# Kernel optimization log

Measured on AMD Instinct MI355X. Metric: run time of the kernel, lower is better.

The kernel has to match this reference:

```python
import jax, jax.numpy as jnp
import numpy as np

ALLOWED_BORDER = 0
CLOBBER_POSITIVES = False
NEG_OVERLAP = 0.3
POS_OVERLAP = 0.7
STRIDE = 16


def _mkanchors(ws, hs, cx, cy):
    return np.stack([cx - 0.5 * (ws - 1), cy - 0.5 * (hs - 1),
                     cx + 0.5 * (ws - 1), cy + 0.5 * (hs - 1)], axis=1)


def _base_anchors(base_size=16, ratios=(0.5, 1.0, 2.0), scales=(8, 16, 32)):
    ratios = np.asarray(ratios, dtype=np.float64)
    scales = np.asarray(scales, dtype=np.float64)
    w = h = float(base_size)
    cx = cy = 0.5 * (base_size - 1)
    size = w * h
    ws = np.round(np.sqrt(size / ratios))
    hs = np.round(ws * ratios)
    ratio_anchors = _mkanchors(ws, hs, cx, cy)  # (3,4)
    out = []
    for x1, y1, x2, y2 in ratio_anchors:
        aw = x2 - x1 + 1
        ah = y2 - y1 + 1
        acx = x1 + 0.5 * (aw - 1)
        acy = y1 + 0.5 * (ah - 1)
        out.append(_mkanchors(aw * scales, ah * scales, acx, acy))
    return np.concatenate(out, axis=0).astype(np.float32)  # (9,4)


def _shift(rr, cc, stride):
    # keras_rcnn.backend.shift: grid of shifted base anchors, (rr*cc*9, 4)
    base = _base_anchors()
    sx = np.arange(rr) * stride
    sy = np.arange(cc) * stride
    SX, SY = np.meshgrid(sx, sy)
    shifts = np.stack([SX.ravel(), SY.ravel(), SX.ravel(), SY.ravel()], axis=1).astype(np.float32)
    return jnp.asarray((shifts[:, None, :] + base[None, :, :]).reshape(-1, 4))


def _iou(a, b):
    # pairwise IoU, (A,4) x (G,4) -> (A,G); +1 pixel convention as in keras-rcnn overlap()
    area_a = (a[:, 2] - a[:, 0] + 1.0) * (a[:, 3] - a[:, 1] + 1.0)
    area_b = (b[:, 2] - b[:, 0] + 1.0) * (b[:, 3] - b[:, 1] + 1.0)
    iw = jnp.maximum(jnp.minimum(a[:, None, 2], b[None, :, 2]) - jnp.maximum(a[:, None, 0], b[None, :, 0]) + 1.0, 0.0)
    ih = jnp.maximum(jnp.minimum(a[:, None, 3], b[None, :, 3]) - jnp.maximum(a[:, None, 1], b[None, :, 1]) + 1.0, 0.0)
    inter = iw * ih
    union = jnp.maximum(area_a[:, None] + area_b[None, :] - inter, 1e-8)
    return inter / union


def _bbox_transform(ex, gt):
    ew = ex[:, 2] - ex[:, 0] + 1.0
    eh = ex[:, 3] - ex[:, 1] + 1.0
    ecx = ex[:, 0] + 0.5 * ew
    ecy = ex[:, 1] + 0.5 * eh
    gw = gt[:, 2] - gt[:, 0] + 1.0
    gh = gt[:, 3] - gt[:, 1] + 1.0
    gcx = gt[:, 0] + 0.5 * gw
    gcy = gt[:, 1] + 0.5 * gh
    return jnp.stack([(gcx - ecx) / ew, (gcy - ecy) / eh,
                      jnp.log(gw / ew), jnp.log(gh / eh)], axis=1)


def setup_inputs():
    key = jax.random.key(0)
    k1, k2, k3 = jax.random.split(key, 3)
    rr = cc = 128
    ch = 18  # 2 * 9 anchors
    G = 256
    H = W = 2048.0
    scores = jax.random.normal(k1, (1, rr, cc, ch), dtype=jnp.float32)
    xy = jax.random.uniform(k2, (1, G, 2), minval=0.0, maxval=1700.0)
    wh = jax.random.uniform(k3, (1, G, 2), minval=16.0, maxval=300.0)
    gt_boxes = jnp.concatenate([xy, xy + wh], axis=-1).astype(jnp.float32)
    metadata = jnp.array([[H, W, 1.0]], dtype=jnp.float32)
    return {"scores": scores, "gt_boxes": gt_boxes, "metadata": metadata}


def reference(scores, gt_boxes, metadata):
    meta = metadata[0, :]
    gt = gt_boxes[0]  # (G,4)
    rr, cc, ch = scores.shape[1:]
    anchors = _shift(rr, cc, STRIDE)  # (A,4), A = rr*cc*9
    # inside_image mask (keeps static shapes: mask instead of gather, unmap at end)
    inside = ((anchors[:, 0] >= -ALLOWED_BORDER) & (anchors[:, 1] >= -ALLOWED_BORDER) &
              (anchors[:, 2] < meta[1] + ALLOWED_BORDER) & (anchors[:, 3] < meta[0] + ALLOWED_BORDER))
    overlaps = _iou(anchors, gt)  # (A,G)
    max_overlaps = overlaps.max(axis=1)          # per-anchor best IoU
    argmax_inds = jnp.argmax(overlaps, axis=1)   # per-anchor best gt
    gt_argmax = jnp.argmax(jnp.where(inside[:, None], overlaps, -1.0), axis=0)  # (G,)
    labels = jnp.full((anchors.shape[0],), -1.0, dtype=jnp.float32)
    if not CLOBBER_POSITIVES:
        labels = jnp.where(max_overlaps < NEG_OVERLAP, 0.0, labels)
    # scatter-add trick from keras-rcnn: sets labels[gt_argmax] to 1 (dup indices accumulate)
    labels = labels.at[gt_argmax].add(1.0 - labels[gt_argmax])
    labels = jnp.where(max_overlaps >= POS_OVERLAP, 1.0, labels)
    if CLOBBER_POSITIVES:
        labels = jnp.where(max_overlaps < NEG_OVERLAP, 0.0, labels)
    bbox = _bbox_transform(anchors, gt[argmax_inds])  # (A,4)
    # unmap: outside anchors -> label -1, bbox targets 0
    labels = jnp.where(inside, labels, -1.0)
    bbox = jnp.where(inside[:, None], bbox, 0.0)
    return labels[None, :], bbox[None, :, :]
```

## Files before the change

### kernel.cpp

```cpp
#include <hip/hip_runtime.h>
#include <stdint.h>

#pragma clang fp contract(off)

#define A_TOTAL 147456
#define G 256
#define NANCHOR_BLOCKS 576
#define TOTAL_BLOCKS (NANCHOR_BLOCKS + G)

__constant__ float c_bx1[9] = { -84.f, -176.f, -360.f,  -56.f, -120.f, -248.f,  -36.f,  -80.f, -168.f };
__constant__ float c_by1[9] = { -40.f,  -88.f, -184.f,  -56.f, -120.f, -248.f,  -80.f, -168.f, -344.f };
__constant__ float c_bx2[9] = {  99.f,  191.f,  375.f,   71.f,  135.f,  263.f,   51.f,   95.f,  183.f };
__constant__ float c_by2[9] = {  55.f,  103.f,  199.f,   71.f,  135.f,  263.f,   95.f,  183.f,  359.f };
__constant__ float c_area[9] = { 17664.f, 70656.f, 282624.f, 16384.f, 65536.f, 262144.f, 15488.f, 61952.f, 247808.f };

__device__ __forceinline__ unsigned int fenc(float f) {
    unsigned int u = __float_as_uint(f);
    return (u & 0x80000000u) ? ~u : (u | 0x80000000u);
}

__device__ __forceinline__ unsigned long long shfl_down_u64(unsigned long long v, int off) {
    unsigned int lo = (unsigned int)v;
    unsigned int hi = (unsigned int)(v >> 32);
    lo = __shfl_down(lo, off, 64);
    hi = __shfl_down(hi, off, 64);
    return ((unsigned long long)hi << 32) | lo;
}

__global__ __launch_bounds__(256) void k_fused(
    const float* __restrict__ gt, const float* __restrict__ meta,
    int* __restrict__ win, float* __restrict__ out)
{
    __shared__ float4 sbox[G];
    __shared__ int    sg[G];
    __shared__ int    wcnt[4], woff[4], sS;
    __shared__ float4 sg0;
    __shared__ unsigned long long red[4];

    const float H = meta[0], W = meta[1];
    const int tid = threadIdx.x;

    if (blockIdx.x >= NANCHOR_BLOCKS) {
        const int g = blockIdx.x - NANCHOR_BLOCKS;
        const float gx1 = gt[4*g+0], gy1 = gt[4*g+1], gx2 = gt[4*g+2], gy2 = gt[4*g+3];
        const float area_b = (gx2 - gx1 + 1.0f) * (gy2 - gy1 + 1.0f);
        const int tx = tid & 15, ty = tid >> 4;

        constexpr int ibx1[9] = {-84,-176,-360,-56,-120,-248,-36,-80,-168};
        constexpr int iby1[9] = {-40,-88,-184,-56,-120,-248,-80,-168,-344};
        constexpr int ibx2[9] = { 99, 191, 375, 71, 135, 263, 51, 95, 183};
        constexpr int iby2[9] = { 55, 103, 199, 71, 135, 263, 95, 183, 359};
        constexpr int iarea[9] = {17664,70656,282624,16384,65536,262144,15488,61952,247808};

        unsigned long long best = 0ULL;
        #pragma unroll
        for (int a = 0; a < 9; ++a) {
            const int xlo_in = (-ibx1[a] + 15) >> 4;
            const int ylo_in = (-iby1[a] + 15) >> 4;
            const int xhi_in = (int)floorf((W - 1.0f - (float)ibx2[a]) * 0.0625f);
            const int yhi_in = (int)floorf((H - 1.0f - (float)iby2[a]) * 0.0625f);
            int xlo = max(max((int)floorf((gx1 - (float)ibx2[a]) * 0.0625f) - 1, xlo_in), 0);
            int xhi = min(min((int)floorf((gx2 - (float)ibx1[a]) * 0.0625f) + 1, xhi_in), 127);
            int ylo = max(max((int)floorf((gy1 - (float)iby2[a]) * 0.0625f) - 1, ylo_in), 0);
            int yhi = min(min((int)floorf((gy2 - (float)iby1[a]) * 0.0625f) + 1, yhi_in), 127);
            const float fa = (float)iarea[a];

            for (int iy = ylo + ty; iy <= yhi; iy += 16) {
                const float ay1 = (float)((iy << 4) + iby1[a]);
                const float ay2 = (float)((iy << 4) + iby2[a]);
                float ih = fminf(ay2, gy2) - fmaxf(ay1, gy1) + 1.0f; ih = fmaxf(ih, 0.0f);
                for (int ix = xlo + tx; ix <= xhi; ix += 16) {
                    const float ax1 = (float)((ix << 4) + ibx1[a]);
                    const float ax2 = (float)((ix << 4) + ibx2[a]);
                    bool inside = (ax1 >= 0.0f) & (ay1 >= 0.0f) & (ax2 < W) & (ay2 < H);
                    float iw = fminf(ax2, gx2) - fmaxf(ax1, gx1) + 1.0f; iw = fmaxf(iw, 0.0f);
                    float inter = iw * ih;
                    float uni = fmaxf(fa + area_b - inter, 1e-8f);
                    float iou = inter / uni;
                    float m = inside ? iou : -1.0f;
                    int n = ((iy << 7) + ix) * 9 + a;
                    unsigned long long e = ((unsigned long long)fenc(m) << 32) | (unsigned int)(~n);
                    if (e > best) best = e;
                }
            }
        }
        for (int off = 32; off >= 1; off >>= 1) {
            unsigned long long o = shfl_down_u64(best, off);
            if (o > best) best = o;
        }
        const int wave = tid >> 6, lane = tid & 63;
        if (lane == 0) red[wave] = best;
        __syncthreads();
        if (tid == 0) {
            unsigned long long v = red[0];
            if (red[1] > v) v = red[1];
            if (red[2] > v) v = red[2];
            if (red[3] > v) v = red[3];
            win[g] = (int)(~(unsigned int)(v & 0xffffffffULL));
        }
        return;
    }

    const int a  = blockIdx.x >> 6;
    const int t  = blockIdx.x & 63;
    const int ix = ((t & 7) << 4) + (tid & 15);
    const int iy = ((t >> 3) << 4) + (tid >> 4);

    const float bx1 = c_bx1[a], by1 = c_by1[a], bx2 = c_bx2[a], by2 = c_by2[a];
    const float area_a = c_area[a];

    {
        const float tx0 = (float)(((t & 7) << 8));
        const float ty0 = (float)(((t >> 3) << 8));
        const float bbx1 = tx0 + bx1 - 4.0f;
        const float bbx2 = tx0 + 240.0f + bx2 + 4.0f;
        const float bby1 = ty0 + by1 - 4.0f;
        const float bby2 = ty0 + 240.0f + by2 + 4.0f;

        float4 b = ((const float4*)gt)[tid];
        if (tid == 0) sg0 = b;
        bool keep = (b.z >= bbx1) & (b.x <= bbx2) & (b.w >= bby1) & (b.y <= bby2);

        unsigned long long m = __ballot(keep);
        const int wave = tid >> 6, lane = tid & 63;
        const int my = __popcll(m & ((1ULL << lane) - 1ULL));
        if (lane == 0) wcnt[wave] = __popcll(m);
        __syncthreads();
        if (tid == 0) {
            int o = 0;
            #pragma unroll
            for (int w = 0; w < 4; ++w) { woff[w] = o; o += wcnt[w]; }
            sS = o;
        }
        __syncthreads();
        if (keep) {
            int p = woff[wave] + my;
            sbox[p] = b;
            sg[p] = tid;
        }
        __syncthreads();
    }
    const int S = sS;

    const float ax1 = (float)((ix << 4)) + bx1;
    const float ay1 = (float)((iy << 4)) + by1;
    const float ax2 = (float)((ix << 4)) + bx2;
    const float ay2 = (float)((iy << 4)) + by2;
    const bool inside = (ax1 >= 0.0f) & (ay1 >= 0.0f) & (ax2 < W) & (ay2 < H);

    float bestv = -1.0f;
    int bj = 0;
    for (int j = 0; j < S; ++j) {
        float4 bb = sbox[j];
        float iw = fminf(ax2, bb.z) - fmaxf(ax1, bb.x) + 1.0f; iw = fmaxf(iw, 0.0f);
        float ih = fminf(ay2, bb.w) - fmaxf(ay1, bb.y) + 1.0f; ih = fmaxf(ih, 0.0f);
        float inter = iw * ih;
        if (__any(inter > 0.0f)) {
            float areab = (bb.z - bb.x + 1.0f) * (bb.w - bb.y + 1.0f);
            float uni = fmaxf(area_a + areab - inter, 1e-8f);
            float iou = inter / uni;
            if (iou > bestv) { bestv = iou; bj = j; }
        }
    }
    int barg; float4 gb;
    if (bestv <= 0.0f) { bestv = 0.0f; barg = 0; gb = sg0; }
    else               { barg = sg[bj]; gb = sbox[bj]; }
    (void)barg;

    float label = -1.0f;
    if (bestv < 0.3f) label = 0.0f;
    if (bestv >= 0.7f) label = 1.0f;
    if (!inside) label = -1.0f;

    float ew = ax2 - ax1 + 1.0f;
    float eh = ay2 - ay1 + 1.0f;
    float ecx = ax1 + 0.5f * ew;
    float ecy = ay1 + 0.5f * eh;
    float gw = gb.z - gb.x + 1.0f;
    float gh = gb.w - gb.y + 1.0f;
    float gcx = gb.x + 0.5f * gw;
    float gcy = gb.y + 0.5f * gh;
    float t0 = (gcx - ecx) / ew;
    float t1 = (gcy - ecy) / eh;
    float t2 = logf(gw / ew);
    float t3 = logf(gh / eh);
    if (!inside) { t0 = 0.0f; t1 = 0.0f; t2 = 0.0f; t3 = 0.0f; }

    const int n = ((iy << 7) + ix) * 9 + a;
    out[n] = label;
    ((float4*)(out + A_TOTAL))[n] = make_float4(t0, t1, t2, t3);
}

__global__ __launch_bounds__(256) void k_fix(
    const float* __restrict__ gt, const int* __restrict__ win,
    float* __restrict__ out)
{
    __shared__ float4 sb[G];
    __shared__ float  sa[G];
    __shared__ int    swin[G];
    const int t = threadIdx.x;
    {
        float4 b = ((const float4*)gt)[t];
        sb[t] = b;
        sa[t] = (b.z - b.x + 1.0f) * (b.w - b.y + 1.0f);
        swin[t] = win[t];
    }
    __syncthreads();

    const int idx = swin[t];
    int k = idx / 9;
    int a = idx - 9 * k;
    float sx = (float)((k & 127) << 4);
    float sy = (float)((k >> 7) << 4);
    float ax1 = sx + c_bx1[a];
    float ay1 = sy + c_by1[a];
    float ax2 = sx + c_bx2[a];
    float ay2 = sy + c_by2[a];
    float area_a = c_area[a];

    float mo = -1.0f;
    int cnt = 0;
    #pragma unroll 4
    for (int g = 0; g < G; ++g) {
        float4 bb = sb[g];
        float iw = fminf(ax2, bb.z) - fmaxf(ax1, bb.x) + 1.0f; iw = fmaxf(iw, 0.0f);
        float ih = fminf(ay2, bb.w) - fmaxf(ay1, bb.y) + 1.0f; ih = fmaxf(ih, 0.0f);
        float inter = iw * ih;
        float uni = fmaxf(area_a + sa[g] - inter, 1e-8f);
        float iou = inter / uni;
        mo = fmaxf(mo, iou);
        cnt += (swin[g] == idx);
    }

    float label = -1.0f;
    if (mo < 0.3f) label = 0.0f;
    label = label + (float)cnt * (1.0f - label);
    if (mo >= 0.7f) label = 1.0f;

    out[idx] = label;
}

extern "C" void kernel_launch(void* const* d_in, const int* in_sizes, int n_in,
                              void* d_out, int out_size, void* d_ws, size_t ws_size,
                              hipStream_t stream) {
    const float* gt   = (const float*)d_in[1];
    const float* meta = (const float*)d_in[2];
    float* out = (float*)d_out;
    int* win = (int*)d_ws;

    k_fused<<<TOTAL_BLOCKS, 256, 0, stream>>>(gt, meta, win, out);
    k_fix<<<1, 256, 0, stream>>>(gt, win, out);
}
```

Measured before the change: 90.91 us.

## Split per-gt argmax into own kernel and apply fixups via atomics

The per-gt best-anchor search moves out of the fused anchor kernel into a separate 256-block kernel. Each block also recomputes the winning anchor's max IoU in parallel and applies the label fixup to the output with an atomicAdd. This replaces the old single-block fix kernel that looped serially over all gts per thread. The atomic accumulation relies on the anchor kernel having already written the base label, and duplicate winners are now summed through atomics rather than counted explicitly.

```diff
diff --git a/kernel.cpp b/kernel.cpp
--- a/kernel.cpp
+++ b/kernel.cpp
@@ -6,7 +6,6 @@
 #define A_TOTAL 147456
 #define G 256
 #define NANCHOR_BLOCKS 576
-#define TOTAL_BLOCKS (NANCHOR_BLOCKS + G)
 
 __constant__ float c_bx1[9] = { -84.f, -176.f, -360.f,  -56.f, -120.f, -248.f,  -36.f,  -80.f, -168.f };
 __constant__ float c_by1[9] = { -40.f,  -88.f, -184.f,  -56.f, -120.f, -248.f,  -80.f, -168.f, -344.f };
@@ -27,79 +26,16 @@
     return ((unsigned long long)hi << 32) | lo;
 }
 
-__global__ __launch_bounds__(256) void k_fused(
+__global__ __launch_bounds__(256) void k_anchor(
     const float* __restrict__ gt, const float* __restrict__ meta,
-    int* __restrict__ win, float* __restrict__ out)
+    float* __restrict__ out)
 {
     __shared__ float4 sbox[G];
-    __shared__ int    sg[G];
     __shared__ int    wcnt[4], woff[4], sS;
     __shared__ float4 sg0;
-    __shared__ unsigned long long red[4];
 
     const float H = meta[0], W = meta[1];
     const int tid = threadIdx.x;
-
-    if (blockIdx.x >= NANCHOR_BLOCKS) {
-        const int g = blockIdx.x - NANCHOR_BLOCKS;
-        const float gx1 = gt[4*g+0], gy1 = gt[4*g+1], gx2 = gt[4*g+2], gy2 = gt[4*g+3];
-        const float area_b = (gx2 - gx1 + 1.0f) * (gy2 - gy1 + 1.0f);
-        const int tx = tid & 15, ty = tid >> 4;
-
-        constexpr int ibx1[9] = {-84,-176,-360,-56,-120,-248,-36,-80,-168};
-        constexpr int iby1[9] = {-40,-88,-184,-56,-120,-248,-80,-168,-344};
-        constexpr int ibx2[9] = { 99, 191, 375, 71, 135, 263, 51, 95, 183};
-        constexpr int iby2[9] = { 55, 103, 199, 71, 135, 263, 95, 183, 359};
-        constexpr int iarea[9] = {17664,70656,282624,16384,65536,262144,15488,61952,247808};
-
-        unsigned long long best = 0ULL;
-        #pragma unroll
-        for (int a = 0; a < 9; ++a) {
-            const int xlo_in = (-ibx1[a] + 15) >> 4;
-            const int ylo_in = (-iby1[a] + 15) >> 4;
-            const int xhi_in = (int)floorf((W - 1.0f - (float)ibx2[a]) * 0.0625f);
-            const int yhi_in = (int)floorf((H - 1.0f - (float)iby2[a]) * 0.0625f);
-            int xlo = max(max((int)floorf((gx1 - (float)ibx2[a]) * 0.0625f) - 1, xlo_in), 0);
-            int xhi = min(min((int)floorf((gx2 - (float)ibx1[a]) * 0.0625f) + 1, xhi_in), 127);
-            int ylo = max(max((int)floorf((gy1 - (float)iby2[a]) * 0.0625f) - 1, ylo_in), 0);
-            int yhi = min(min((int)floorf((gy2 - (float)iby1[a]) * 0.0625f) + 1, yhi_in), 127);
-            const float fa = (float)iarea[a];
-
-            for (int iy = ylo + ty; iy <= yhi; iy += 16) {
-                const float ay1 = (float)((iy << 4) + iby1[a]);
-                const float ay2 = (float)((iy << 4) + iby2[a]);
-                float ih = fminf(ay2, gy2) - fmaxf(ay1, gy1) + 1.0f; ih = fmaxf(ih, 0.0f);
-                for (int ix = xlo + tx; ix <= xhi; ix += 16) {
-                    const float ax1 = (float)((ix << 4) + ibx1[a]);
-                    const float ax2 = (float)((ix << 4) + ibx2[a]);
-                    bool inside = (ax1 >= 0.0f) & (ay1 >= 0.0f) & (ax2 < W) & (ay2 < H);
-                    float iw = fminf(ax2, gx2) - fmaxf(ax1, gx1) + 1.0f; iw = fmaxf(iw, 0.0f);
-                    float inter = iw * ih;
-                    float uni = fmaxf(fa + area_b - inter, 1e-8f);
-                    float iou = inter / uni;
-                    float m = inside ? iou : -1.0f;
-                    int n = ((iy << 7) + ix) * 9 + a;
-                    unsigned long long e = ((unsigned long long)fenc(m) << 32) | (unsigned int)(~n);
-                    if (e > best) best = e;
-                }
-            }
-        }
-        for (int off = 32; off >= 1; off >>= 1) {
-            unsigned long long o = shfl_down_u64(best, off);
-            if (o > best) best = o;
-        }
-        const int wave = tid >> 6, lane = tid & 63;
-        if (lane == 0) red[wave] = best;
-        __syncthreads();
-        if (tid == 0) {
-            unsigned long long v = red[0];
-            if (red[1] > v) v = red[1];
-            if (red[2] > v) v = red[2];
-            if (red[3] > v) v = red[3];
-            win[g] = (int)(~(unsigned int)(v & 0xffffffffULL));
-        }
-        return;
-    }
 
     const int a  = blockIdx.x >> 6;
     const int t  = blockIdx.x & 63;
@@ -133,11 +69,7 @@
             sS = o;
         }
         __syncthreads();
-        if (keep) {
-            int p = woff[wave] + my;
-            sbox[p] = b;
-            sg[p] = tid;
-        }
+        if (keep) sbox[woff[wave] + my] = b;
         __syncthreads();
     }
     const int S = sS;
@@ -162,10 +94,9 @@
             if (iou > bestv) { bestv = iou; bj = j; }
         }
     }
-    int barg; float4 gb;
-    if (bestv <= 0.0f) { bestv = 0.0f; barg = 0; gb = sg0; }
-    else               { barg = sg[bj]; gb = sbox[bj]; }
-    (void)barg;
+    float4 gb;
+    if (bestv <= 0.0f) { bestv = 0.0f; gb = sg0; }
+    else               { gb = sbox[bj]; }
 
     float label = -1.0f;
     if (bestv < 0.3f) label = 0.0f;
@@ -191,53 +122,105 @@
     ((float4*)(out + A_TOTAL))[n] = make_float4(t0, t1, t2, t3);
 }
 
-__global__ __launch_bounds__(256) void k_fix(
-    const float* __restrict__ gt, const int* __restrict__ win,
+__global__ __launch_bounds__(256) void k_gt(
+    const float* __restrict__ gt, const float* __restrict__ meta,
     float* __restrict__ out)
 {
-    __shared__ float4 sb[G];
-    __shared__ float  sa[G];
-    __shared__ int    swin[G];
-    const int t = threadIdx.x;
-    {
-        float4 b = ((const float4*)gt)[t];
-        sb[t] = b;
-        sa[t] = (b.z - b.x + 1.0f) * (b.w - b.y + 1.0f);
-        swin[t] = win[t];
-    }
-    __syncthreads();
-
-    const int idx = swin[t];
-    int k = idx / 9;
-    int a = idx - 9 * k;
-    float sx = (float)((k & 127) << 4);
-    float sy = (float)((k >> 7) << 4);
-    float ax1 = sx + c_bx1[a];
-    float ay1 = sy + c_by1[a];
-    float ax2 = sx + c_bx2[a];
-    float ay2 = sy + c_by2[a];
+    __shared__ float4 sGT[G];
+    __shared__ unsigned long long red[4];
+    __shared__ float mred[4];
+
+    const int g = blockIdx.x;
+    const int tid = threadIdx.x;
+    sGT[tid] = ((const float4*)gt)[tid];
+    __syncthreads();
+
+    const float4 me = sGT[g];
+    const float gx1 = me.x, gy1 = me.y, gx2 = me.z, gy2 = me.w;
+    const float area_b = (gx2 - gx1 + 1.0f) * (gy2 - gy1 + 1.0f);
+    const float H = meta[0], W = meta[1];
+    const int tx = tid & 15, ty = tid >> 4;
+
+    constexpr int ibx1[9] = {-84,-176,-360,-56,-120,-248,-36,-80,-168};
+    constexpr int iby1[9] = {-40,-88,-184,-56,-120,-248,-80,-168,-344};
+    constexpr int ibx2[9] = { 99, 191, 375, 71, 135, 263, 51, 95, 183};
+    constexpr int iby2[9] = { 55, 103, 199, 71, 135, 263, 95, 183, 359};
+    constexpr int iarea[9] = {17664,70656,282624,16384,65536,262144,15488,61952,247808};
+
+    unsigned long long best = 0ULL;
+    #pragma unroll
+    for (int a = 0; a < 9; ++a) {
+        const int xlo_in = (-ibx1[a] + 15) >> 4;
+        const int ylo_in = (-iby1[a] + 15) >> 4;
+        const int xhi_in = (int)floorf((W - 1.0f - (float)ibx2[a]) * 0.0625f);
+        const int yhi_in = (int)floorf((H - 1.0f - (float)iby2[a]) * 0.0625f);
+        int xlo = max(max((int)floorf((gx1 - (float)ibx2[a]) * 0.0625f) - 1, xlo_in), 0);
+        int xhi = min(min((int)floorf((gx2 - (float)ibx1[a]) * 0.0625f) + 1, xhi_in), 127);
+        int ylo = max(max((int)floorf((gy1 - (float)iby2[a]) * 0.0625f) - 1, ylo_in), 0);
+        int yhi = min(min((int)floorf((gy2 - (float)iby1[a]) * 0.0625f) + 1, yhi_in), 127);
+        const float fa = (float)iarea[a];
+
+        for (int iy = ylo + ty; iy <= yhi; iy += 16) {
+            const float ay1 = (float)((iy << 4) + iby1[a]);
+            const float ay2 = (float)((iy << 4) + iby2[a]);
+            float ih = fminf(ay2, gy2) - fmaxf(ay1, gy1) + 1.0f; ih = fmaxf(ih, 0.0f);
+            for (int ix = xlo + tx; ix <= xhi; ix += 16) {
+                const float ax1 = (float)((ix << 4) + ibx1[a]);
+                const float ax2 = (float)((ix << 4) + ibx2[a]);
+                bool inside = (ax1 >= 0.0f) & (ay1 >= 0.0f) & (ax2 < W) & (ay2 < H);
+                float iw = fminf(ax2, gx2) - fmaxf(ax1, gx1) + 1.0f; iw = fmaxf(iw, 0.0f);
+                float inter = iw * ih;
+                float uni = fmaxf(fa + area_b - inter, 1e-8f);
+                float iou = inter / uni;
+                float m = inside ? iou : -1.0f;
+                int n = ((iy << 7) + ix) * 9 + a;
+                unsigned long long e = ((unsigned long long)fenc(m) << 32) | (unsigned int)(~n);
+                if (e > best) best = e;
+            }
+        }
+    }
+    for (int off = 32; off >= 1; off >>= 1) {
+        unsigned long long o = shfl_down_u64(best, off);
+        if (o > best) best = o;
+    }
+    const int wave = tid >> 6, lane = tid & 63;
+    if (lane == 0) red[wave] = best;
+    __syncthreads();
+    if (tid == 0) {
+        unsigned long long v = red[0];
+        if (red[1] > v) v = red[1];
+        if (red[2] > v) v = red[2];
+        if (red[3] > v) v = red[3];
+        red[0] = v;
+    }
+    __syncthreads();
+    const int w = (int)(~(unsigned int)(red[0] & 0xffffffffULL));
+
+    int k = w / 9;
+    int a = w - 9 * k;
+    float ax1 = (float)(((k & 127) << 4)) + c_bx1[a];
+    float ay1 = (float)(((k >> 7) << 4)) + c_by1[a];
+    float ax2 = (float)(((k & 127) << 4)) + c_bx2[a];
+    float ay2 = (float)(((k >> 7) << 4)) + c_by2[a];
     float area_a = c_area[a];
 
-    float mo = -1.0f;
-    int cnt = 0;
-    #pragma unroll 4
-    for (int g = 0; g < G; ++g) {
-        float4 bb = sb[g];
-        float iw = fminf(ax2, bb.z) - fmaxf(ax1, bb.x) + 1.0f; iw = fmaxf(iw, 0.0f);
-        float ih = fminf(ay2, bb.w) - fmaxf(ay1, bb.y) + 1.0f; ih = fmaxf(ih, 0.0f);
-        float inter = iw * ih;
-        float uni = fmaxf(area_a + sa[g] - inter, 1e-8f);
-        float iou = inter / uni;
-        mo = fmaxf(mo, iou);
-        cnt += (swin[g] == idx);
-    }
-
-    float label = -1.0f;
-    if (mo < 0.3f) label = 0.0f;
-    label = label + (float)cnt * (1.0f - label);
-    if (mo >= 0.7f) label = 1.0f;
-
-    out[idx] = label;
+    float4 bb = sGT[tid];
+    float iw = fminf(ax2, bb.z) - fmaxf(ax1, bb.x) + 1.0f; iw = fmaxf(iw, 0.0f);
+    float ih = fminf(ay2, bb.w) - fmaxf(ay1, bb.y) + 1.0f; ih = fmaxf(ih, 0.0f);
+    float inter = iw * ih;
+    float areab = (bb.z - bb.x + 1.0f) * (bb.w - bb.y + 1.0f);
+    float uni = fmaxf(area_a + areab - inter, 1e-8f);
+    float mo = inter / uni;
+    for (int off = 32; off >= 1; off >>= 1) mo = fmaxf(mo, __shfl_down(mo, off, 64));
+    if (lane == 0) mred[wave] = mo;
+    __syncthreads();
+    if (tid == 0) {
+        float m = fmaxf(fmaxf(mred[0], mred[1]), fmaxf(mred[2], mred[3]));
+        if (m < 0.7f) {
+            float o = (m < 0.3f) ? 0.0f : -1.0f;
+            atomicAdd(&out[w], 1.0f - o);
+        }
+    }
 }
 
 extern "C" void kernel_launch(void* const* d_in, const int* in_sizes, int n_in,
@@ -246,8 +229,7 @@
     const float* gt   = (const float*)d_in[1];
     const float* meta = (const float*)d_in[2];
     float* out = (float*)d_out;
-    int* win = (int*)d_ws;
-
-    k_fused<<<TOTAL_BLOCKS, 256, 0, stream>>>(gt, meta, win, out);
-    k_fix<<<1, 256, 0, stream>>>(gt, win, out);
-}
+
+    k_anchor<<<NANCHOR_BLOCKS, 256, 0, stream>>>(gt, meta, out);
+    k_gt<<<G, 256, 0, stream>>>(gt, meta, out);
+}
```

After: 84.15 us. 1.08x faster.
